# Performance work log

Measured on AMD Instinct MI355X. Metric: run time of the kernel, lower is better.

## Reference

```python
import jax, jax.numpy as jnp
import numpy as np

UNITS = 256


def setup_inputs() -> dict:
    key = jax.random.key(0)
    ks = jax.random.split(key, 9)
    B, H, W, C = 8, 64, 64, UNITS
    x = jax.random.normal(ks[0], (B, H, W, C), dtype=jnp.float32)
    # 1x1 Conv2D == per-pixel linear: weight [C_in, C_out], bias [C_out]
    def lin(k):
        return jax.random.normal(k, (C, UNITS), dtype=jnp.float32) * (2.0 / C) ** 0.5
    return {
        "x": x,
        "wq": lin(ks[1]), "bq": jnp.zeros((UNITS,), jnp.float32),
        "wk": lin(ks[2]), "bk": jnp.zeros((UNITS,), jnp.float32),
        "wv": lin(ks[3]), "bv": jnp.zeros((UNITS,), jnp.float32),
        "wp": lin(ks[4]), "bp": jnp.zeros((UNITS,), jnp.float32),
    }


def reference(x, wq, bq, wk, bk, wv, bv, wp, bp):
    B, H, W, C = x.shape
    N = H * W
    scale = jnp.asarray(UNITS, jnp.float32) ** -0.5
    xf = x.reshape(B, N, C)  # 1x1 conv == matmul over channels
    q = xf @ wq + bq
    k = xf @ wk + bk
    v = xf @ wv + bv
    # (b,h,w,c)x(b,H,W,c)->(b,h,w,H,W) flattened to (b,N,N)
    scores = jnp.einsum('bnc,bmc->bnm', q, k) * scale
    attn = jax.nn.softmax(scores, axis=-1)
    out = jnp.einsum('bnm,bmc->bnc', attn, v)
    proj = out @ wp + bp
    return x + proj.reshape(B, H, W, UNITS)
```

## Files before the change

kernel.cpp:

```cpp
#include <hip/hip_runtime.h>


typedef _Float16 half8 __attribute__((ext_vector_type(8)));
typedef _Float16 half4 __attribute__((ext_vector_type(4)));
typedef float f32x4 __attribute__((ext_vector_type(4)));
typedef float f32x16 __attribute__((ext_vector_type(16)));
typedef unsigned int u32x4 __attribute__((ext_vector_type(4)));
typedef unsigned int u32x2 __attribute__((ext_vector_type(2)));

#define MFMA16(a, b, c) __builtin_amdgcn_mfma_f32_16x16x32_f16((a), (b), (c), 0, 0, 0)
#define MFMA32(a, b, c) __builtin_amdgcn_mfma_f32_32x32x16_f16((a), (b), (c), 0, 0, 0)

#if __has_builtin(__builtin_amdgcn_exp2f)
#define EXP2(x) __builtin_amdgcn_exp2f(x)
#else
#define EXP2(x) exp2f(x)
#endif

#define QSCALE 0.09016843898f
#define ESHIFT 11.5415603f

__device__ __forceinline__ void lds_load16(const void* g, void* l) {
    __builtin_amdgcn_global_load_lds(
        (const __attribute__((address_space(1))) unsigned int*)g,
        (__attribute__((address_space(3))) unsigned int*)l, 16, 0, 0);
}

__global__ __launch_bounds__(256)
void wt_prep(const float* __restrict__ w0, const float* __restrict__ w1,
             const float* __restrict__ w2, const float* __restrict__ w3,
             _Float16* __restrict__ outw)
{
    __shared__ _Float16 sT[64 * 72];
    const int z = blockIdx.z;
    const float* W = (z == 0) ? w0 : (z == 1) ? w1 : (z == 2) ? w2 : w3;
    _Float16* O = outw + z * 65536;
    const int kb = blockIdx.x * 64, nb = blockIdx.y * 64;
    const int t = threadIdx.x;
    const int r = t >> 4, c4 = (t & 15) * 4;
#pragma unroll
    for (int i = 0; i < 4; ++i) {
        f32x4 ld = *(const f32x4*)(W + (size_t)(kb + r + i * 16) * 256 + nb + c4);
#pragma unroll
        for (int j = 0; j < 4; ++j) sT[(c4 + j) * 72 + r + i * 16] = (_Float16)ld[j];
    }
    __syncthreads();
#pragma unroll
    for (int i = 0; i < 4; ++i) {
        int n = r + i * 16;
        *(u32x2*)&O[(size_t)(nb + n) * 256 + kb + c4] = *(const u32x2*)&sT[n * 72 + c4];
    }
}

__global__ __launch_bounds__(256)
void qkv_gemm(const float* __restrict__ x, const _Float16* __restrict__ wt,
              const float* __restrict__ bq, const float* __restrict__ bk,
              const float* __restrict__ bv,
              _Float16* __restrict__ qo, _Float16* __restrict__ ko,
              _Float16* __restrict__ vo)
{
    __shared__ _Float16 smem[12800];

    const int tid  = threadIdx.x;
    const int w    = tid >> 6;
    const int lane = tid & 63;
    const int quad = lane >> 4;
    const int l16  = lane & 15;
    const int m0   = blockIdx.x * 128;
    const int n0   = blockIdx.y * 64;
    const int rA = tid >> 1, cA = (tid & 1) << 4;
    const int rB = tid >> 2, cB = (tid & 3) << 3;

    const float* ap = x + (size_t)(m0 + rA) * 256 + cA;
    f32x4 a0 = *(const f32x4*)ap,       a1 = *(const f32x4*)(ap + 4);
    f32x4 a2 = *(const f32x4*)(ap + 8), a3 = *(const f32x4*)(ap + 12);
    u32x4 bst[3];
#pragma unroll
    for (int o = 0; o < 3; ++o)
        bst[o] = *(const u32x4*)(wt + o * 65536 + (size_t)(n0 + rB) * 256 + cB);

    f32x4 zero4 = {0.f, 0.f, 0.f, 0.f};
    f32x4 acc[3][8];
#pragma unroll
    for (int o = 0; o < 3; ++o)
#pragma unroll
        for (int mt = 0; mt < 8; ++mt) acc[o][mt] = zero4;

    for (int it = 0; it < 8; ++it) {
        __syncthreads();
        half8 t0, t1;
#pragma unroll
        for (int j = 0; j < 4; ++j) {
            t0[j] = (_Float16)a0[j]; t0[j + 4] = (_Float16)a1[j];
            t1[j] = (_Float16)a2[j]; t1[j + 4] = (_Float16)a3[j];
        }
        *(half8*)&smem[rA * 40 + cA]     = t0;
        *(half8*)&smem[rA * 40 + cA + 8] = t1;
#pragma unroll
        for (int o = 0; o < 3; ++o)
            *(u32x4*)&smem[5120 + o * 2560 + rB * 40 + cB] = bst[o];
        __syncthreads();
        if (it < 7) {
            int k0 = (it + 1) * 32;
            const float* ap2 = x + (size_t)(m0 + rA) * 256 + k0 + cA;
            a0 = *(const f32x4*)ap2;       a1 = *(const f32x4*)(ap2 + 4);
            a2 = *(const f32x4*)(ap2 + 8); a3 = *(const f32x4*)(ap2 + 12);
#pragma unroll
            for (int o = 0; o < 3; ++o)
                bst[o] = *(const u32x4*)(wt + o * 65536 + (size_t)(n0 + rB) * 256 + k0 + cB);
        }
        half8 af[8];
#pragma unroll
        for (int mt = 0; mt < 8; ++mt)
            af[mt] = *(const half8*)&smem[(mt * 16 + l16) * 40 + quad * 8];
#pragma unroll
        for (int o = 0; o < 3; ++o) {
            half8 bf = *(const half8*)&smem[5120 + o * 2560 + (16 * w + l16) * 40 + quad * 8];
#pragma unroll
            for (int mt = 0; mt < 8; ++mt)
                acc[o][mt] = MFMA16(af[mt], bf, acc[o][mt]);
        }
    }

    const int col = n0 + 16 * w + l16;
#pragma unroll
    for (int mt = 0; mt < 8; ++mt) {
#pragma unroll
        for (int reg = 0; reg < 4; ++reg) {
            int row = m0 + 16 * mt + quad * 4 + reg;
            qo[(size_t)row * 256 + col] = (_Float16)((acc[0][mt][reg] + bq[col]) * QSCALE);
            ko[(size_t)row * 256 + col] = (_Float16)(acc[1][mt][reg] + bk[col]);
        }
    }
    __syncthreads();
    _Float16* sT = smem;
#pragma unroll
    for (int mt = 0; mt < 8; ++mt)
#pragma unroll
        for (int reg = 0; reg < 4; ++reg)
            sT[(16 * w + l16) * 136 + 16 * mt + quad * 4 + reg] =
                (_Float16)(acc[2][mt][reg] + bv[col]);
    __syncthreads();
    int ch = tid >> 2, po = (tid & 3) << 5;
    int bb = m0 >> 12, pix = m0 & 4095;
    _Float16* dst = vo + (size_t)bb * 1048576 + (size_t)(n0 + ch) * 4096 + pix + po;
#pragma unroll
    for (int i = 0; i < 4; ++i)
        *(u32x4*)(dst + i * 8) = *(const u32x4*)&sT[ch * 136 + po + i * 8];
}

__global__ __launch_bounds__(256)
void proj_gemm(const _Float16* __restrict__ opart, const float* __restrict__ lpart,
               const _Float16* __restrict__ Wt, const float* __restrict__ bias,
               const float* __restrict__ resid, float* __restrict__ out)
{
    __shared__ _Float16 smem[7680];
    _Float16* sB = smem + 5120;

    const int tid  = threadIdx.x;
    const int w    = tid >> 6;
    const int lane = tid & 63;
    const int quad = lane >> 4;
    const int l16  = lane & 15;
    const int m0   = blockIdx.x * 128;
    const int n0   = blockIdx.y * 64;
    const int rA = tid >> 1, cA = (tid & 1) << 4;
    const int rB = tid >> 2, cB = (tid & 3) << 3;

    const _Float16* o1p = opart;
    const _Float16* o2p = opart + 8388608;
    const int row = m0 + rA;
    const float inv = 1.0f / (lpart[row] + lpart[32768 + row]);

    u32x4 a1v = *(const u32x4*)(o1p + (size_t)row * 256 + cA);
    u32x4 a1w = *(const u32x4*)(o1p + (size_t)row * 256 + cA + 8);
    u32x4 a2v = *(const u32x4*)(o2p + (size_t)row * 256 + cA);
    u32x4 a2w = *(const u32x4*)(o2p + (size_t)row * 256 + cA + 8);
    u32x4 bst = *(const u32x4*)(Wt + (size_t)(n0 + rB) * 256 + cB);

    f32x4 zero4 = {0.f, 0.f, 0.f, 0.f};
    f32x4 acc[2][4];
#pragma unroll
    for (int m = 0; m < 2; ++m)
#pragma unroll
        for (int nt = 0; nt < 4; ++nt) acc[m][nt] = zero4;

    for (int it = 0; it < 8; ++it) {
        __syncthreads();
        {
            half8 h1 = *(half8*)&a1v, h2 = *(half8*)&a2v, t;
#pragma unroll
            for (int j = 0; j < 8; ++j)
                t[j] = (_Float16)(((float)h1[j] + (float)h2[j]) * inv);
            *(half8*)&smem[rA * 40 + cA] = t;
            half8 g1 = *(half8*)&a1w, g2 = *(half8*)&a2w, u;
#pragma unroll
            for (int j = 0; j < 8; ++j)
                u[j] = (_Float16)(((float)g1[j] + (float)g2[j]) * inv);
            *(half8*)&smem[rA * 40 + cA + 8] = u;
        }
        *(u32x4*)&sB[rB * 40 + cB] = bst;
        __syncthreads();
        if (it < 7) {
            int k0 = (it + 1) * 32;
            a1v = *(const u32x4*)(o1p + (size_t)row * 256 + k0 + cA);
            a1w = *(const u32x4*)(o1p + (size_t)row * 256 + k0 + cA + 8);
            a2v = *(const u32x4*)(o2p + (size_t)row * 256 + k0 + cA);
            a2w = *(const u32x4*)(o2p + (size_t)row * 256 + k0 + cA + 8);
            bst = *(const u32x4*)(Wt + (size_t)(n0 + rB) * 256 + k0 + cB);
        }
        half8 af[2];
#pragma unroll
        for (int m = 0; m < 2; ++m)
            af[m] = *(const half8*)&smem[((2 * w + m) * 16 + l16) * 40 + quad * 8];
#pragma unroll
        for (int nt = 0; nt < 4; ++nt) {
            half8 bf = *(const half8*)&sB[(nt * 16 + l16) * 40 + quad * 8];
#pragma unroll
            for (int m = 0; m < 2; ++m)
                acc[m][nt] = MFMA16(af[m], bf, acc[m][nt]);
        }
    }
#pragma unroll
    for (int m = 0; m < 2; ++m)
#pragma unroll
        for (int nt = 0; nt < 4; ++nt) {
#pragma unroll
            for (int reg = 0; reg < 4; ++reg) {
                int orow = m0 + (2 * w + m) * 16 + quad * 4 + reg;
                int col = n0 + nt * 16 + l16;
                out[(size_t)orow * 256 + col] =
                    acc[m][nt][reg] + bias[col] + resid[(size_t)orow * 256 + col];
            }
        }
}

__global__ __launch_bounds__(512, 2)
void attn_kernel(const _Float16* __restrict__ q, const _Float16* __restrict__ k,
                 const _Float16* __restrict__ vt, _Float16* __restrict__ opart,
                 float* __restrict__ lpart)
{
    extern __shared__ char smem[];
    char* sKb = smem;
    char* sVb = smem + 32768;

    const int tid  = threadIdx.x;
    const int w    = tid >> 6;
    const int lane = tid & 63;
    const int l31  = lane & 31;
    const int hi   = lane >> 5;
    const int kh   = blockIdx.x & 1;
    const int qg   = (blockIdx.x >> 1) & 15;
    const int b    = blockIdx.x >> 5;

    const _Float16* kb = k  + (size_t)b * 1048576 + (size_t)kh * 524288;
    const _Float16* vb = vt + (size_t)b * 1048576 + kh * 2048;
    const int rowbase = qg * 256 + w * 32;

    half8 qf[16];
    {
        const _Float16* q0 = q + (size_t)(b * 4096 + rowbase + l31) * 256 + hi * 8;
#pragma unroll
        for (int s = 0; s < 16; ++s) qf[s] = *(const half8*)(q0 + s * 16);
    }

    f32x16 o[8];
#pragma unroll
    for (int i = 0; i < 8; ++i)
#pragma unroll
        for (int j = 0; j < 16; ++j) o[i][j] = 0.f;
    float ls = 0.f;

    const int koffL = l31 * 256 + hi * 8;

#pragma unroll
    for (int j = 0; j < 2; ++j) {
        int s = w * 2 + j;
        lds_load16(kb + koffL + s * 16, sKb + s * 1024);
        int ct = s >> 1, ks = s & 1;
        lds_load16(vb + (size_t)(32 * ct + l31) * 4096 + 16 * ks + 8 * hi,
                   sVb + s * 1024);
    }

    for (int kt = 0; kt < 64; ++kt) {
        const int p = kt & 1;
        __syncthreads();

        if (kt < 63) {
            const _Float16* ktb = kb + (size_t)(kt + 1) * 8192;
            const _Float16* vtb = vb + (kt + 1) * 32;
            char* dK = sKb + (1 - p) * 16384;
            char* dV = sVb + (1 - p) * 16384;
#pragma unroll
            for (int j = 0; j < 2; ++j) {
                int s = w * 2 + j;
                lds_load16(ktb + koffL + s * 16, dK + s * 1024);
                int ct = s >> 1, ks = s & 1;
                lds_load16(vtb + (size_t)(32 * ct + l31) * 4096 + 16 * ks + 8 * hi,
                           dV + s * 1024);
            }
        }

        const char* K = sKb + p * 16384;
        const char* V = sVb + p * 16384;

        f32x16 saA, saB;
#pragma unroll
        for (int j = 0; j < 16; ++j) { saA[j] = 0.f; saB[j] = 0.f; }
        __builtin_amdgcn_s_setprio(1);
#pragma unroll
        for (int s = 0; s < 16; s += 2) {
            half8 a0 = *(const half8*)(K + s * 1024 + lane * 16);
            half8 a1 = *(const half8*)(K + (s + 1) * 1024 + lane * 16);
            saA = MFMA32(a0, qf[s], saA);
            saB = MFMA32(a1, qf[s + 1], saB);
        }
        __builtin_amdgcn_s_setprio(0);

        unsigned int c[8];
#pragma unroll
        for (int j = 0; j < 8; ++j) saA[j] += saB[j];
#pragma unroll
        for (int qq = 0; qq < 2; ++qq) {
            float p0 = EXP2(saA[qq * 4 + 0] - ESHIFT);
            float p1 = EXP2(saA[qq * 4 + 1] - ESHIFT);
            float p2 = EXP2(saA[qq * 4 + 2] - ESHIFT);
            float p3 = EXP2(saA[qq * 4 + 3] - ESHIFT);
            ls += (p0 + p1) + (p2 + p3);
            c[2 * qq]     = __builtin_bit_cast(unsigned int,
                                __builtin_amdgcn_cvt_pkrtz(p0, p1));
            c[2 * qq + 1] = __builtin_bit_cast(unsigned int,
                                __builtin_amdgcn_cvt_pkrtz(p2, p3));
        }
        u32x2 s0 = __builtin_amdgcn_permlane32_swap(c[0], c[2], false, false);
        u32x2 s1 = __builtin_amdgcn_permlane32_swap(c[1], c[3], false, false);
        u32x4 w0 = {s0[0], s1[0], s0[1], s1[1]};
        half8 pf0 = __builtin_bit_cast(half8, w0);

        __builtin_amdgcn_s_setprio(1);
#pragma unroll
        for (int ct = 0; ct < 8; ++ct) {
            half8 b0 = *(const half8*)(V + (ct * 2 + 0) * 1024 + lane * 16);
            o[ct] = MFMA32(pf0, b0, o[ct]);
        }
        __builtin_amdgcn_s_setprio(0);

#pragma unroll
        for (int j = 8; j < 16; ++j) saA[j] += saB[j];
#pragma unroll
        for (int qq = 2; qq < 4; ++qq) {
            float p0 = EXP2(saA[qq * 4 + 0] - ESHIFT);
            float p1 = EXP2(saA[qq * 4 + 1] - ESHIFT);
            float p2 = EXP2(saA[qq * 4 + 2] - ESHIFT);
            float p3 = EXP2(saA[qq * 4 + 3] - ESHIFT);
            ls += (p0 + p1) + (p2 + p3);
            c[2 * qq]     = __builtin_bit_cast(unsigned int,
                                __builtin_amdgcn_cvt_pkrtz(p0, p1));
            c[2 * qq + 1] = __builtin_bit_cast(unsigned int,
                                __builtin_amdgcn_cvt_pkrtz(p2, p3));
        }
        u32x2 s2 = __builtin_amdgcn_permlane32_swap(c[4], c[6], false, false);
        u32x2 s3 = __builtin_amdgcn_permlane32_swap(c[5], c[7], false, false);
        u32x4 w1 = {s2[0], s3[0], s2[1], s3[1]};
        half8 pf1 = __builtin_bit_cast(half8, w1);

        __builtin_amdgcn_s_setprio(1);
#pragma unroll
        for (int ct = 0; ct < 8; ++ct) {
            half8 b1 = *(const half8*)(V + (ct * 2 + 1) * 1024 + lane * 16);
            o[ct] = MFMA32(pf1, b1, o[ct]);
        }
        __builtin_amdgcn_s_setprio(0);
    }

    ls += __shfl_xor(ls, 32);
    _Float16* po = opart + (size_t)kh * 8388608 + (size_t)(b * 4096 + rowbase) * 256;
    float* pl = lpart + kh * 32768 + b * 4096 + rowbase;
    if (hi == 0) pl[l31] = ls;
#pragma unroll
    for (int ct = 0; ct < 8; ++ct) {
#pragma unroll
        for (int reg = 0; reg < 16; ++reg) {
            int row = (reg & 3) + 8 * (reg >> 2) + 4 * hi;
            po[(size_t)row * 256 + ct * 32 + l31] = (_Float16)o[ct][reg];
        }
    }
}

extern "C" void kernel_launch(void* const* d_in, const int* in_sizes, int n_in,
                              void* d_out, int out_size, void* d_ws, size_t ws_size,
                              hipStream_t stream) {
    const float* x  = (const float*)d_in[0];
    const float* wq = (const float*)d_in[1];
    const float* bq = (const float*)d_in[2];
    const float* wk = (const float*)d_in[3];
    const float* bk = (const float*)d_in[4];
    const float* wv = (const float*)d_in[5];
    const float* bv = (const float*)d_in[6];
    const float* wp = (const float*)d_in[7];
    const float* bp = (const float*)d_in[8];

    _Float16* qws  = (_Float16*)d_ws;
    _Float16* kws  = qws + 8388608;
    _Float16* vtws = kws + 8388608;
    _Float16* ows  = vtws + 8388608;
    _Float16* wt   = ows + 16777216;
    float*    lws  = (float*)(wt + 262144);

    dim3 blk(256);

    (void)hipFuncSetAttribute((const void*)attn_kernel,
                              hipFuncAttributeMaxDynamicSharedMemorySize, 65536);

    wt_prep<<<dim3(4, 4, 4), blk, 0, stream>>>(wq, wk, wv, wp, wt);
    qkv_gemm<<<dim3(256, 4), blk, 0, stream>>>(x, wt, bq, bk, bv, qws, kws, vtws);
    attn_kernel<<<dim3(256), dim3(512), 65536, stream>>>(qws, kws, vtws, ows, lws);
    proj_gemm<<<dim3(256, 4), blk, 0, stream>>>(ows, lws, wt + 196608, bp, x, (float*)d_out);
}
```

Before: 286.2 us.

## Double-buffer LDS in GEMMs and remap attention blocks for XCD locality

```diff
diff --git a/kernel.cpp b/kernel.cpp
--- a/kernel.cpp
+++ b/kernel.cpp
@@ -59,7 +59,7 @@
               _Float16* __restrict__ qo, _Float16* __restrict__ ko,
               _Float16* __restrict__ vo)
 {
-    __shared__ _Float16 smem[12800];
+    __shared__ _Float16 smem[25600];
 
     const int tid  = threadIdx.x;
     const int w    = tid >> 6;
@@ -87,18 +87,18 @@
         for (int mt = 0; mt < 8; ++mt) acc[o][mt] = zero4;
 
     for (int it = 0; it < 8; ++it) {
-        __syncthreads();
+        _Float16* buf = smem + (it & 1) * 12800;
         half8 t0, t1;
 #pragma unroll
         for (int j = 0; j < 4; ++j) {
             t0[j] = (_Float16)a0[j]; t0[j + 4] = (_Float16)a1[j];
             t1[j] = (_Float16)a2[j]; t1[j + 4] = (_Float16)a3[j];
         }
-        *(half8*)&smem[rA * 40 + cA]     = t0;
-        *(half8*)&smem[rA * 40 + cA + 8] = t1;
+        *(half8*)&buf[rA * 40 + cA]     = t0;
+        *(half8*)&buf[rA * 40 + cA + 8] = t1;
 #pragma unroll
         for (int o = 0; o < 3; ++o)
-            *(u32x4*)&smem[5120 + o * 2560 + rB * 40 + cB] = bst[o];
+            *(u32x4*)&buf[5120 + o * 2560 + rB * 40 + cB] = bst[o];
         __syncthreads();
         if (it < 7) {
             int k0 = (it + 1) * 32;
@@ -112,10 +112,10 @@
         half8 af[8];
 #pragma unroll
         for (int mt = 0; mt < 8; ++mt)
-            af[mt] = *(const half8*)&smem[(mt * 16 + l16) * 40 + quad * 8];
+            af[mt] = *(const half8*)&buf[(mt * 16 + l16) * 40 + quad * 8];
 #pragma unroll
         for (int o = 0; o < 3; ++o) {
-            half8 bf = *(const half8*)&smem[5120 + o * 2560 + (16 * w + l16) * 40 + quad * 8];
+            half8 bf = *(const half8*)&buf[5120 + o * 2560 + (16 * w + l16) * 40 + quad * 8];
 #pragma unroll
             for (int mt = 0; mt < 8; ++mt)
                 acc[o][mt] = MFMA16(af[mt], bf, acc[o][mt]);
@@ -154,8 +154,7 @@
                const _Float16* __restrict__ Wt, const float* __restrict__ bias,
                const float* __restrict__ resid, float* __restrict__ out)
 {
-    __shared__ _Float16 smem[7680];
-    _Float16* sB = smem + 5120;
+    __shared__ _Float16 smem[15360];
 
     const int tid  = threadIdx.x;
     const int w    = tid >> 6;
@@ -186,18 +185,19 @@
         for (int nt = 0; nt < 4; ++nt) acc[m][nt] = zero4;
 
     for (int it = 0; it < 8; ++it) {
-        __syncthreads();
+        _Float16* buf = smem + (it & 1) * 7680;
+        _Float16* sB = buf + 5120;
         {
             half8 h1 = *(half8*)&a1v, h2 = *(half8*)&a2v, t;
 #pragma unroll
             for (int j = 0; j < 8; ++j)
                 t[j] = (_Float16)(((float)h1[j] + (float)h2[j]) * inv);
-            *(half8*)&smem[rA * 40 + cA] = t;
+            *(half8*)&buf[rA * 40 + cA] = t;
             half8 g1 = *(half8*)&a1w, g2 = *(half8*)&a2w, u;
 #pragma unroll
             for (int j = 0; j < 8; ++j)
                 u[j] = (_Float16)(((float)g1[j] + (float)g2[j]) * inv);
-            *(half8*)&smem[rA * 40 + cA + 8] = u;
+            *(half8*)&buf[rA * 40 + cA + 8] = u;
         }
         *(u32x4*)&sB[rB * 40 + cB] = bst;
         __syncthreads();
@@ -212,7 +212,7 @@
         half8 af[2];
 #pragma unroll
         for (int m = 0; m < 2; ++m)
-            af[m] = *(const half8*)&smem[((2 * w + m) * 16 + l16) * 40 + quad * 8];
+            af[m] = *(const half8*)&buf[((2 * w + m) * 16 + l16) * 40 + quad * 8];
 #pragma unroll
         for (int nt = 0; nt < 4; ++nt) {
             half8 bf = *(const half8*)&sB[(nt * 16 + l16) * 40 + quad * 8];
@@ -249,9 +249,12 @@
     const int lane = tid & 63;
     const int l31  = lane & 31;
     const int hi   = lane >> 5;
-    const int kh   = blockIdx.x & 1;
-    const int qg   = (blockIdx.x >> 1) & 15;
-    const int b    = blockIdx.x >> 5;
+    const int bid  = blockIdx.x;
+    const int xcd  = bid & 7, idx = bid >> 3;
+    const int g    = xcd + 8 * (idx & 1);
+    const int qg   = idx >> 1;
+    const int b    = g >> 1;
+    const int kh   = g & 1;
 
     const _Float16* kb = k  + (size_t)b * 1048576 + (size_t)kh * 524288;
     const _Float16* vb = vt + (size_t)b * 1048576 + kh * 2048;
```

Result: slower. 298.0 us (+4.1%).
